# Optimization experiments

Measured on AMD Instinct MI355X. Metric: run time of the kernel, lower is better.

The kernel has to match this reference:

```python
import jax, jax.numpy as jnp
import numpy as np

FEAT_STRIDE = 16
NEG_OV, POS_OV = 0.3, 0.7
RPN_BATCH = 256
NUM_FG = int(0.5 * RPN_BATCH)  # RPN_FG_FRACTION * RPN_BATCHSIZE


def _gen_anchors(base=16, ratios=(0.5, 1.0, 2.0), scales=(4, 8, 16)):
    # 3D extension of the classic generate_anchors: ratio warps w/h, scale multiplies all dims
    ctr = (base - 1) / 2.0
    rows = []
    for r in ratios:
        for s in scales:
            w = base * s * np.sqrt(1.0 / r)
            h = base * s * np.sqrt(r)
            d = float(base * s)
            rows.append([ctr - 0.5 * (w - 1), ctr - 0.5 * (h - 1),
                         ctr + 0.5 * (w - 1), ctr + 0.5 * (h - 1),
                         ctr - 0.5 * (d - 1), ctr + 0.5 * (d - 1)])
    return np.asarray(rows, np.float32)


def setup_inputs() -> dict:
    key = jax.random.key(0)
    ks = jax.random.split(key, 8)
    B, H, W, D, K, A = 2, 48, 48, 24, 20, 9
    cls = jax.random.normal(ks[0], (B, 2 * A, H, W, D), jnp.float32)
    x1 = jax.random.uniform(ks[1], (B, K)) * 600.0
    y1 = jax.random.uniform(ks[2], (B, K)) * 600.0
    z1 = jax.random.uniform(ks[3], (B, K)) * 300.0
    whd = 16.0 + jax.random.uniform(ks[4], (B, K, 3)) * jnp.array([104.0, 104.0, 48.0])
    x2 = jnp.minimum(x1 + whd[..., 0], 767.0)
    y2 = jnp.minimum(y1 + whd[..., 1], 767.0)
    z2 = jnp.minimum(z1 + whd[..., 2], 383.0)
    cid = jax.random.randint(ks[5], (B, K), 1, 4).astype(jnp.float32)
    gt_boxes = jnp.stack([x1, y1, x2, y2, z1, z2, cid], axis=2)
    im_info = jnp.tile(jnp.array([[768.0, 768.0, 384.0]], jnp.float32), (B, 1))
    total = H * W * D * A
    return {
        'rpn_cls_score': cls,
        'gt_boxes': gt_boxes,
        'im_info': im_info,
        'num_boxes': jnp.full((B,), K, jnp.int32),
        'anchors': jnp.asarray(_gen_anchors()),
        'rand_fg': jax.random.uniform(ks[6], (B, total)),
        'rand_bg': jax.random.uniform(ks[7], (B, total)),
    }


def _overlaps(anc, gt):
    # anc: (N,6) [x1,y1,x2,y2,z1,z2]; gt: (B,K,7) -> IoU (B,N,K)
    aw = anc[:, 2] - anc[:, 0] + 1.0
    ah = anc[:, 3] - anc[:, 1] + 1.0
    ad = anc[:, 5] - anc[:, 4] + 1.0
    a_area = aw * ah * ad  # (N,)
    gw = gt[:, :, 2] - gt[:, :, 0] + 1.0
    gh = gt[:, :, 3] - gt[:, :, 1] + 1.0
    gd = gt[:, :, 5] - gt[:, :, 4] + 1.0
    g_area = gw * gh * gd  # (B,K)
    iw = jnp.clip(jnp.minimum(anc[None, :, None, 2], gt[:, None, :, 2]) -
                  jnp.maximum(anc[None, :, None, 0], gt[:, None, :, 0]) + 1.0, 0.0)
    ih = jnp.clip(jnp.minimum(anc[None, :, None, 3], gt[:, None, :, 3]) -
                  jnp.maximum(anc[None, :, None, 1], gt[:, None, :, 1]) + 1.0, 0.0)
    idp = jnp.clip(jnp.minimum(anc[None, :, None, 5], gt[:, None, :, 5]) -
                   jnp.maximum(anc[None, :, None, 4], gt[:, None, :, 4]) + 1.0, 0.0)
    inter = iw * ih * idp
    ov = inter / (a_area[None, :, None] + g_area[:, None, :] - inter)
    gt_zero = (gw == 1.0) & (gh == 1.0) & (gd == 1.0)
    a_zero = (aw == 1.0) & (ah == 1.0) & (ad == 1.0)
    ov = jnp.where(gt_zero[:, None, :], 0.0, ov)
    ov = jnp.where(a_zero[None, :, None], -1.0, ov)
    return ov


def _transform(ex, gt):
    # ex: (N,6); gt: (B,N,6) -> (B,N,6) targets (dx,dy,dz,dw,dh,dd)
    ew = ex[:, 2] - ex[:, 0] + 1.0
    eh = ex[:, 3] - ex[:, 1] + 1.0
    ed = ex[:, 5] - ex[:, 4] + 1.0
    ecx = ex[:, 0] + 0.5 * (ew - 1.0)
    ecy = ex[:, 1] + 0.5 * (eh - 1.0)
    ecz = ex[:, 4] + 0.5 * (ed - 1.0)
    gw = gt[:, :, 2] - gt[:, :, 0] + 1.0
    gh = gt[:, :, 3] - gt[:, :, 1] + 1.0
    gd = gt[:, :, 5] - gt[:, :, 4] + 1.0
    gcx = gt[:, :, 0] + 0.5 * (gw - 1.0)
    gcy = gt[:, :, 1] + 0.5 * (gh - 1.0)
    gcz = gt[:, :, 4] + 0.5 * (gd - 1.0)
    return jnp.stack([(gcx - ecx[None]) / ew[None],
                      (gcy - ecy[None]) / eh[None],
                      (gcz - ecz[None]) / ed[None],
                      jnp.log(gw / ew[None]),
                      jnp.log(gh / eh[None]),
                      jnp.log(gd / ed[None])], axis=2)


def _rank(p):
    # rank of each element when sorted by descending priority, per row
    return jnp.argsort(jnp.argsort(-p, axis=1), axis=1)


def reference(rpn_cls_score, gt_boxes, im_info, num_boxes, anchors, rand_fg, rand_bg):
    B = gt_boxes.shape[0]
    H, W, D = rpn_cls_score.shape[2], rpn_cls_score.shape[3], rpn_cls_score.shape[4]
    A = anchors.shape[0]
    sx = jnp.arange(W, dtype=jnp.float32) * FEAT_STRIDE
    sy = jnp.arange(H, dtype=jnp.float32) * FEAT_STRIDE
    sz = jnp.arange(D, dtype=jnp.float32) * FEAT_STRIDE
    mx, my, mz = jnp.meshgrid(sx, sy, sz, indexing='xy')  # (H,W,D) each
    shifts = jnp.stack([mx.ravel(), my.ravel(), mx.ravel(), my.ravel(), mz.ravel(), mz.ravel()], axis=1)
    all_anchors = (anchors[None, :, :] + shifts[:, None, :]).reshape(-1, 6)  # (total,6)
    total = all_anchors.shape[0]
    inside = ((all_anchors[:, 0] >= 0) & (all_anchors[:, 1] >= 0) & (all_anchors[:, 4] >= 0) &
              (all_anchors[:, 2] < im_info[0, 1]) & (all_anchors[:, 3] < im_info[0, 0]) &
              (all_anchors[:, 5] < im_info[0, 2]))  # (total,)

    ov = _overlaps(all_anchors, gt_boxes)                       # (B,total,K)
    ov_m = jnp.where(inside[None, :, None], ov, -1.0)           # mask outside anchors
    max_ov = ov_m.max(axis=2)
    argmax_ov = jnp.argmax(ov_m, axis=2)                        # (B,total)

    labels = jnp.full((B, total), -1.0, jnp.float32)
    ins = inside[None, :]
    labels = jnp.where(ins & (max_ov < NEG_OV), 0.0, labels)
    gt_max = ov_m.max(axis=1)                                   # (B,K)
    gt_max = jnp.where(gt_max == 0.0, 1e-5, gt_max)
    tie = jnp.sum(ov_m == gt_max[:, None, :], axis=2) > 0
    labels = jnp.where(ins & tie, 1.0, labels)
    labels = jnp.where(ins & (max_ov >= POS_OV), 1.0, labels)

    # fg subsampling: randomly keep at most NUM_FG positives per image
    fg = labels == 1.0
    rk = _rank(jnp.where(fg, rand_fg, -1.0))
    labels = jnp.where(fg & (rk >= NUM_FG), -1.0, labels)
    # bg subsampling: keep RPN_BATCH - num_fg negatives per image
    num_bg = RPN_BATCH - jnp.sum(labels == 1.0, axis=1)         # (B,)
    bg = labels == 0.0
    rkb = _rank(jnp.where(bg, rand_bg, -1.0))
    labels = jnp.where(bg & (rkb >= num_bg[:, None]), -1.0, labels)

    assigned = jnp.take_along_axis(gt_boxes, argmax_ov[:, :, None], axis=1)  # (B,total,7)
    bbox_targets = _transform(all_anchors, assigned[:, :, :6])
    bbox_targets = jnp.where(inside[None, :, None], bbox_targets, 0.0)

    in_w = jnp.where(labels == 1.0, 1.0, 0.0)                   # RPN_BBOX_INSIDE_WEIGHTS[0]=1
    # replicate original bug: weights from the LAST image's example count
    num_examples = jnp.sum(labels[-1] >= 0.0).astype(jnp.float32)
    w = 1.0 / num_examples
    out_w = jnp.where(labels == 1.0, w, jnp.where(labels == 0.0, w, 0.0))

    labels_o = labels.reshape(B, H, W, D, A).transpose(0, 4, 1, 2, 3).reshape(B, 1, A * H * D, W)
    bt_o = bbox_targets.reshape(B, H, W, D, A * 6).transpose(0, 4, 1, 2, 3)
    iw_o = jnp.broadcast_to(in_w[:, :, None], (B, total, 6)).reshape(B, H, W, D, 6 * A).transpose(0, 4, 1, 2, 3)
    ow_o = jnp.broadcast_to(out_w[:, :, None], (B, total, 6)).reshape(B, H, W, D, 6 * A).transpose(0, 4, 1, 2, 3)
    return labels_o, bt_o, iw_o, ow_o
```

## Files before the change

### kernel.cpp

```cpp
#include <hip/hip_runtime.h>
#include <math.h>

#define BB 2
#define HH 48
#define WW 48
#define DD 24
#define KK 20
#define AA 9
#define TOTAL (HH*WW*DD*AA)
#define SPAT (HH*WW*DD)
#define OUT0N (BB*TOTAL)
#define CH 54
#define NB 4096
#define CAPB 256
#define FG_QUOTA 128
#define RPN_B 256
#define STRIDE_F 16.0f

#define O_REC    0
#define O_GTMAX  (OUT0N)
#define O_HIST   (O_GTMAX + BB*KK)
#define O_CUT    (O_HIST + 4*NB)
#define O_W      (O_CUT + 16)
#define O_LIST   (O_W + 1)

__device__ __forceinline__ unsigned enc_f(float f){
  unsigned u = __float_as_uint(f);
  return (u & 0x80000000u) ? ~u : (u | 0x80000000u);
}
__device__ __forceinline__ float dec_f(unsigned u){
  return (u & 0x80000000u) ? __uint_as_float(u & 0x7FFFFFFFu) : __uint_as_float(~u);
}
#define ENC_NEG1 0x407FFFFFu

__device__ __forceinline__ float iou_pre(float ax1,float ay1,float ax2,float ay2,
                                         float az1,float az2,float a_area,
                                         const float* g){
  #pragma clang fp contract(off)
  float iw = fminf(ax2,g[2]) - fmaxf(ax1,g[0]) + 1.0f; iw = fmaxf(iw,0.0f);
  float ih = fminf(ay2,g[3]) - fmaxf(ay1,g[1]) + 1.0f; ih = fmaxf(ih,0.0f);
  float id = fminf(az2,g[5]) - fmaxf(az1,g[4]) + 1.0f; id = fmaxf(id,0.0f);
  float inter = iw*ih*id;
  if (inter <= 0.0f) return 0.0f;
  return inter / ((a_area + g[6]) - inter);
}

__device__ __forceinline__ void gt_derive(const float* gt7, float* g8){
  #pragma clang fp contract(off)
  float gw = gt7[2]-gt7[0]+1.0f, gh = gt7[3]-gt7[1]+1.0f, gd = gt7[5]-gt7[4]+1.0f;
  g8[0]=gt7[0]; g8[1]=gt7[1]; g8[2]=gt7[2]; g8[3]=gt7[3];
  g8[4]=gt7[4]; g8[5]=gt7[5]; g8[6]=gw*gh*gd; g8[7]=0.0f;
}

#define GM_SB 108
__global__ void __launch_bounds__(256) k_gtmax(const float* __restrict__ gt,
    const float* __restrict__ anc, const float* __restrict__ imi,
    unsigned* __restrict__ ws){
  __shared__ float s_gd[KK*8];
  __shared__ float s_a6[6];
  __shared__ float s_im[3];
  __shared__ unsigned s_max[KK];
  int tid = threadIdx.x;
  int a = blockIdx.y;
  int b = blockIdx.z;
  if (b == 0 && a == 0 && blockIdx.x < 16){
    int base = blockIdx.x*256 + tid;
    #pragma unroll
    for (int j=0;j<4;j++) ws[O_HIST + j*NB + base] = 0u;
  }
  if (tid < KK) gt_derive(&gt[(b*KK+tid)*7], &s_gd[tid*8]);
  if (tid < 6)  s_a6[tid] = anc[a*6+tid];
  if (tid < 3)  s_im[tid] = imi[tid];
  if (tid < KK) s_max[tid] = ENC_NEG1;
  __syncthreads();
  float rmax[KK];
  #pragma unroll
  for (int k=0;k<KK;k++) rmax[k] = -1.0f;
  int s0 = blockIdx.x*256 + tid;
  #pragma unroll
  for (int j=0; j<2; j++){
    int s = s0 + j*(GM_SB*256);
    int d = s % DD; int s2 = s / DD;
    int w = s2 % WW; int h = s2 / WW;
    float fx = w*STRIDE_F, fy = h*STRIDE_F, fz = d*STRIDE_F;
    float ax1=s_a6[0]+fx, ay1=s_a6[1]+fy, ax2=s_a6[2]+fx;
    float ay2=s_a6[3]+fy, az1=s_a6[4]+fz, az2=s_a6[5]+fz;
    bool inside = (ax1>=0.f)&&(ay1>=0.f)&&(az1>=0.f)&&
                  (ax2<s_im[1])&&(ay2<s_im[0])&&(az2<s_im[2]);
    if (inside){
      #pragma clang fp contract(off)
      float aw = ax2-ax1+1.0f, ah = ay2-ay1+1.0f, ad = az2-az1+1.0f;
      float a_area = aw*ah*ad;
      #pragma unroll
      for (int k=0;k<KK;k++)
        rmax[k] = fmaxf(rmax[k], iou_pre(ax1,ay1,ax2,ay2,az1,az2,a_area,&s_gd[k*8]));
    }
  }
  #pragma unroll
  for (int k=0;k<KK;k++){
    float v = rmax[k];
    for (int off=32; off>0; off>>=1) v = fmaxf(v, __shfl_down(v, off, 64));
    if ((tid & 63) == 0) atomicMax(&s_max[k], enc_f(v));
  }
  __syncthreads();
  if (tid < KK) atomicMax(&ws[O_GTMAX + b*KK + tid], s_max[tid]);
}

__global__ void __launch_bounds__(256) k_label(const float* __restrict__ gt,
    const float* __restrict__ anc, const float* __restrict__ imi,
    const float* __restrict__ rfg, const float* __restrict__ rbg,
    unsigned* __restrict__ ws){
  __shared__ float s_gd[BB*KK*8];
  __shared__ float s_anc[AA*6];
  __shared__ float s_im[3];
  __shared__ float s_gm[BB*KK];
  int tid = threadIdx.x;
  int t = blockIdx.x*256 + tid;
  int d = t % DD; int r1 = t/DD;
  int w = r1 % WW; int r2 = r1/WW;
  int h = r2 % HH; int r3 = r2/HH;
  int a = r3 % AA; int b = r3/AA;
  int i = ((h*WW+w)*DD + d)*AA + a;
  float rf = rfg[b*TOTAL + i];
  float rb = rbg[b*TOTAL + i];
  if (tid < BB*KK) gt_derive(&gt[tid*7], &s_gd[tid*8]);
  for (int j=tid; j<AA*6; j+=256) s_anc[j] = anc[j];
  if (tid<3) s_im[tid] = imi[tid];
  if (tid<BB*KK){ float g = dec_f(ws[O_GTMAX+tid]); if (g==0.0f) g = 1e-5f; s_gm[tid]=g; }
  __syncthreads();
  float fx=w*STRIDE_F, fy=h*STRIDE_F, fz=d*STRIDE_F;
  float ax1=s_anc[a*6+0]+fx, ay1=s_anc[a*6+1]+fy, ax2=s_anc[a*6+2]+fx;
  float ay2=s_anc[a*6+3]+fy, az1=s_anc[a*6+4]+fz, az2=s_anc[a*6+5]+fz;
  bool inside = (ax1>=0.f)&&(ay1>=0.f)&&(az1>=0.f)&&
                (ax2<s_im[1])&&(ay2<s_im[0])&&(az2<s_im[2]);
  float L = -1.0f;
  int am = 0;
  if (inside){
    #pragma clang fp contract(off)
    float aw = ax2-ax1+1.0f, ah = ay2-ay1+1.0f, ad = az2-az1+1.0f;
    float a_area = aw*ah*ad;
    float mv = -2.0f; bool tie = false;
    #pragma unroll
    for (int k=0;k<KK;k++){
      float ov = iou_pre(ax1,ay1,ax2,ay2,az1,az2,a_area,&s_gd[(b*KK+k)*8]);
      if (ov > mv){ mv = ov; am = k; }
      tie = tie || (ov == s_gm[b*KK+k]);
    }
    if (mv < 0.3f) L = 0.0f;
    if (tie)       L = 1.0f;
    if (mv >= 0.7f) L = 1.0f;
  }
  unsigned code = (L==1.0f) ? 2u : ((L==0.0f) ? 1u : 0u);
  unsigned bucket = 0;
  if (code){
    int fl = (code==1u ? 2 : 0) + b;
    float r = (code==1u) ? rb : rf;
    bucket = (unsigned)min(NB-1, (int)(r*(float)NB));
    unsigned pos = atomicAdd(&ws[O_HIST + fl*NB + bucket], 1u);
    if (pos < CAPB) ((int*)ws)[O_LIST + ((fl*NB + (int)bucket)<<8) + pos] = i;
  }
  ws[O_REC + t] = code | ((unsigned)am<<2) | (bucket<<7);
}

__global__ void __launch_bounds__(256) k_cuts(unsigned* __restrict__ ws){
  int fl = blockIdx.x; int tid = threadIdx.x;
  int b = fl & 1; int isbg = fl >> 1;
  const int CHK = NB/256;
  __shared__ unsigned ps[256];
  __shared__ unsigned s_fg;
  if (tid == 0) s_fg = 0u;
  __syncthreads();
  int hi = NB - CHK*tid;
  unsigned hv[CHK];
  #pragma unroll
  for (int e=0; e<CHK; e++) hv[e] = ws[O_HIST + fl*NB + (hi-CHK+e)];
  unsigned part = 0;
  #pragma unroll
  for (int e=0; e<CHK; e++) part += hv[e];
  if (isbg){
    unsigned fv[CHK];
    #pragma unroll
    for (int e=0; e<CHK; e++) fv[e] = ws[O_HIST + b*NB + tid*CHK + e];
    unsigned pf = 0;
    #pragma unroll
    for (int e=0; e<CHK; e++) pf += fv[e];
    atomicAdd(&s_fg, pf);
  }
  ps[tid] = part;
  __syncthreads();
  for (int off=1; off<256; off<<=1){
    unsigned v = (tid>=off) ? ps[tid-off] : 0u;
    __syncthreads();
    ps[tid] += v;
    __syncthreads();
  }
  unsigned N = ps[255];
  unsigned excl = ps[tid] - part;
  unsigned F = isbg ? s_fg : N;
  int quota = isbg ? (RPN_B - (int)min(F, (unsigned)FG_QUOTA)) : FG_QUOTA;
  if (fl == 3 && tid == 0){
    int fgk = min((int)F, FG_QUOTA);
    int bgk = min((int)N, RPN_B - fgk);
    ((float*)ws)[O_W] = 1.0f / (float)(fgk + bgk);
  }
  int* cut = (int*)&ws[O_CUT + fl*4];
  if ((int)N <= quota){
    if (tid==0){ cut[0] = -1; cut[1] = 0; cut[2] = quota; cut[3] = 0; }
    return;
  }
  unsigned cum = excl;
  #pragma unroll
  for (int e=CHK-1; e>=0; e--){
    int bk = hi-CHK+e;
    unsigned c = hv[e];
    if (c > 0u && (unsigned)(quota-1) >= cum && (unsigned)(quota-1) < cum + c){
      cut[0] = bk; cut[1] = (int)cum; cut[2] = quota; cut[3] = (int)c;
    }
    cum += c;
  }
}

__global__ void __launch_bounds__(256) k_out(const float* __restrict__ gt,
    const float* __restrict__ anc, const float* __restrict__ imi,
    const float* __restrict__ rfg, const float* __restrict__ rbg,
    float* __restrict__ out, const unsigned* __restrict__ ws){
  __shared__ float s_gt[BB*KK*7];
  __shared__ float s_anc[AA*6];
  __shared__ float s_im[3];
  __shared__ float s_w;
  int tid = threadIdx.x;
  for (int j=tid; j<BB*KK*7; j+=256) s_gt[j] = gt[j];
  for (int j=tid; j<AA*6; j+=256) s_anc[j] = anc[j];
  if (tid<3) s_im[tid] = imi[tid];
  if (tid==0) s_w = ((const float*)ws)[O_W];
  __syncthreads();
  int t4 = (blockIdx.x*256 + tid)*4;
  int d0 = t4 % DD; int r1=t4/DD;
  int w = r1 % WW; int r2 = r1/WW;
  int h = r2 % HH; int r3 = r2/HH;
  int a = r3 % AA; int b = r3/AA;
  const uint4 rec4 = *reinterpret_cast<const uint4*>(&ws[O_REC + t4]);
  unsigned recs[4] = {rec4.x, rec4.y, rec4.z, rec4.w};
  float sw = s_w;
  float fx=w*STRIDE_F, fy=h*STRIDE_F;
  float ax1=s_anc[a*6+0]+fx, ay1=s_anc[a*6+1]+fy;
  float ax2=s_anc[a*6+2]+fx, ay2=s_anc[a*6+3]+fy;
  float L4[4], iw4[4], ow4[4], btv[6][4];
  #pragma unroll
  for (int dd=0; dd<4; dd++){
    int d = d0 + dd;
    unsigned rec = recs[dd];
    unsigned code = rec & 3u;
    int am = (int)((rec>>2) & 31u);
    int bucket = (int)((rec>>7) & 4095u);
    float L = (code==2u) ? 1.0f : ((code==1u) ? 0.0f : -1.0f);
    if (code){
      int isbg = (code==1u);
      int fl = isbg*2 + b;
      const int* cut = (const int*)&ws[O_CUT + fl*4];
      int cutb = cut[0];
      if (cutb >= 0){
        if (bucket < cutb) L = -1.0f;
        else if (bucket == cutb){
          int rank_base = cut[1], quota = cut[2];
          int n = min(cut[3], CAPB);
          int i = ((h*WW+w)*DD + d)*AA + a;
          const float* ra = isbg ? rbg : rfg;
          float ri = ra[b*TOTAL + i];
          const int* lst = (const int*)ws + O_LIST + ((fl*NB + cutb)<<8);
          int cnt = 0;
          for (int e=0; e<n; e++){
            int jj = lst[e];
            float rj = ra[b*TOTAL + jj];
            cnt += (rj > ri) || (rj == ri && jj < i);
          }
          if (rank_base + cnt >= quota) L = -1.0f;
        }
      }
    }
    float fz = d*STRIDE_F;
    float az1 = s_anc[a*6+4]+fz, az2 = s_anc[a*6+5]+fz;
    bool inside = (ax1>=0.f)&&(ay1>=0.f)&&(az1>=0.f)&&
                  (ax2<s_im[1])&&(ay2<s_im[0])&&(az2<s_im[2]);
    float bt[6] = {0.f,0.f,0.f,0.f,0.f,0.f};
    if (inside){
      const float* g = &s_gt[(b*KK + am)*7];
      float ew=ax2-ax1+1.f, eh=ay2-ay1+1.f, ed=az2-az1+1.f;
      float ecx=ax1+0.5f*(ew-1.f), ecy=ay1+0.5f*(eh-1.f), ecz=az1+0.5f*(ed-1.f);
      float gw=g[2]-g[0]+1.f, gh=g[3]-g[1]+1.f, gd=g[5]-g[4]+1.f;
      float gcx=g[0]+0.5f*(gw-1.f), gcy=g[1]+0.5f*(gh-1.f), gcz=g[4]+0.5f*(gd-1.f);
      bt[0]=(gcx-ecx)/ew; bt[1]=(gcy-ecy)/eh; bt[2]=(gcz-ecz)/ed;
      bt[3]=logf(gw/ew);  bt[4]=logf(gh/eh);  bt[5]=logf(gd/ed);
    }
    L4[dd] = L;
    iw4[dd] = (L==1.0f) ? 1.0f : 0.0f;
    ow4[dd] = (L==1.0f || L==0.0f) ? sw : 0.0f;
    #pragma unroll
    for (int c=0; c<6; c++) btv[c][dd] = bt[c];
  }
  *reinterpret_cast<float4*>(&out[t4]) = make_float4(L4[0],L4[1],L4[2],L4[3]);
  int sp = (h*WW + w)*DD + d0;
  float* out1 = out + OUT0N;
  float* out2 = out1 + BB*CH*SPAT;
  float* out3 = out2 + BB*CH*SPAT;
  int basech = (b*CH + a*6)*SPAT + sp;
  float4 iwv = make_float4(iw4[0],iw4[1],iw4[2],iw4[3]);
  float4 owv = make_float4(ow4[0],ow4[1],ow4[2],ow4[3]);
  #pragma unroll
  for (int c=0; c<6; c++){
    int off = basech + c*SPAT;
    *reinterpret_cast<float4*>(&out1[off]) = make_float4(btv[c][0],btv[c][1],btv[c][2],btv[c][3]);
    *reinterpret_cast<float4*>(&out2[off]) = iwv;
    *reinterpret_cast<float4*>(&out3[off]) = owv;
  }
}

extern "C" void kernel_launch(void* const* d_in, const int* in_sizes, int n_in,
                              void* d_out, int out_size, void* d_ws, size_t ws_size,
                              hipStream_t stream) {
  (void)in_sizes; (void)n_in; (void)out_size; (void)ws_size;
  const float* gt  = (const float*)d_in[1];
  const float* imi = (const float*)d_in[2];
  const float* anc = (const float*)d_in[4];
  const float* rfg = (const float*)d_in[5];
  const float* rbg = (const float*)d_in[6];
  float* out = (float*)d_out;
  unsigned* ws = (unsigned*)d_ws;
  int nb = (OUT0N + 255)/256;
  int nb4 = (OUT0N + 1023)/1024;
  hipMemsetAsync((char*)d_ws + (size_t)O_GTMAX*4, 0, BB*KK*4, stream);
  k_gtmax <<<dim3(GM_SB, AA, BB), dim3(256), 0, stream>>>(gt, anc, imi, ws);
  k_label <<<dim3(nb), dim3(256), 0, stream>>>(gt, anc, imi, rfg, rbg, ws);
  k_cuts  <<<dim3(4), dim3(256), 0, stream>>>(ws);
  k_out   <<<dim3(nb4), dim3(256), 0, stream>>>(gt, anc, imi, rfg, rbg, out, ws);
}
```

Before: 191.2 us.

## Fuse all four stages into one cooperative kernel with grid syncs

Replaces the memset plus four kernel launches with a single cooperative kernel of 972 blocks. Each thread handles four anchors and keeps its records in registers across grid.sync barriers, so the intermediate record array is no longer written and read back. The per-GT max now uses per-block partials instead of global atomics, and the IoU is computed twice inside the fused kernel. The cost is several grid-wide barriers, a 256-register budget from launch_bounds(256,4), and a fallback to the old launches if the cooperative launch fails.

Result: slower. 592.4 us (+209.9%).

```diff
diff --git a/kernel.cpp b/kernel.cpp
--- a/kernel.cpp
+++ b/kernel.cpp
@@ -1,5 +1,8 @@
 #include <hip/hip_runtime.h>
+#include <hip/hip_cooperative_groups.h>
 #include <math.h>
+
+namespace cg = cooperative_groups;
 
 #define BB 2
 #define HH 48
@@ -16,6 +19,8 @@
 #define FG_QUOTA 128
 #define RPN_B 256
 #define STRIDE_F 16.0f
+#define GRID 972
+#define NBLK_B 486
 
 #define O_REC    0
 #define O_GTMAX  (OUT0N)
@@ -23,6 +28,7 @@
 #define O_CUT    (O_HIST + 4*NB)
 #define O_W      (O_CUT + 16)
 #define O_LIST   (O_W + 1)
+#define O_PART   (O_LIST + 4*NB*CAPB)
 
 __device__ __forceinline__ unsigned enc_f(float f){
   unsigned u = __float_as_uint(f);
@@ -50,6 +56,256 @@
   float gw = gt7[2]-gt7[0]+1.0f, gh = gt7[3]-gt7[1]+1.0f, gd = gt7[5]-gt7[4]+1.0f;
   g8[0]=gt7[0]; g8[1]=gt7[1]; g8[2]=gt7[2]; g8[3]=gt7[3];
   g8[4]=gt7[4]; g8[5]=gt7[5]; g8[6]=gw*gh*gd; g8[7]=0.0f;
+}
+
+__global__ void __launch_bounds__(256, 4) k_fused(
+    const float* __restrict__ gt, const float* __restrict__ anc,
+    const float* __restrict__ imi, const float* __restrict__ rfg,
+    const float* __restrict__ rbg, float* __restrict__ out,
+    unsigned* __restrict__ ws){
+  cg::grid_group grid = cg::this_grid();
+  float* ws_f = (float*)ws;
+  __shared__ float s_gd[BB*KK*8];
+  __shared__ float s_anc[AA*6];
+  __shared__ float s_im[3];
+  __shared__ float s_gm[BB*KK];
+  __shared__ float s_red[4][KK];
+  __shared__ unsigned ps[256];
+  __shared__ unsigned s_fg;
+  __shared__ float s_w;
+  int tid = threadIdx.x;
+  int blk = blockIdx.x;
+  int wv = tid >> 6, ln = tid & 63;
+  int t4 = (blk*256 + tid)*4;
+  int d0 = t4 % DD; int r1 = t4/DD;
+  int w  = r1 % WW; int r2 = r1/WW;
+  int h  = r2 % HH; int r3 = r2/HH;
+  int a  = r3 % AA; int b  = r3/AA;
+  if (tid < BB*KK) gt_derive(&gt[tid*7], &s_gd[tid*8]);
+  for (int j=tid; j<AA*6; j+=256) s_anc[j] = anc[j];
+  if (tid < 3) s_im[tid] = imi[tid];
+  if (blk < 16){
+    int base = blk*256 + tid;
+    #pragma unroll
+    for (int j=0;j<4;j++) ws[O_HIST + j*NB + base] = 0u;
+  }
+  __syncthreads();
+  float fx = w*STRIDE_F, fy = h*STRIDE_F;
+  float ax1=s_anc[a*6+0]+fx, ay1=s_anc[a*6+1]+fy;
+  float ax2=s_anc[a*6+2]+fx, ay2=s_anc[a*6+3]+fy;
+  float anz1 = s_anc[a*6+4], anz2 = s_anc[a*6+5];
+  bool okxy = (ax1>=0.f)&&(ay1>=0.f)&&(ax2<s_im[1])&&(ay2<s_im[0]);
+  float rmax[KK];
+  #pragma unroll
+  for (int k=0;k<KK;k++) rmax[k] = -1.0f;
+  #pragma unroll
+  for (int dd=0; dd<4; dd++){
+    float fz = (float)(d0+dd)*STRIDE_F;
+    float az1 = anz1+fz, az2 = anz2+fz;
+    bool inside = okxy && (az1>=0.f) && (az2<s_im[2]);
+    if (inside){
+      #pragma clang fp contract(off)
+      float aw = ax2-ax1+1.0f, ah = ay2-ay1+1.0f, ad = az2-az1+1.0f;
+      float a_area = aw*ah*ad;
+      #pragma unroll
+      for (int k=0;k<KK;k++)
+        rmax[k] = fmaxf(rmax[k], iou_pre(ax1,ay1,ax2,ay2,az1,az2,a_area,&s_gd[(b*KK+k)*8]));
+    }
+  }
+  #pragma unroll
+  for (int k=0;k<KK;k++){
+    float v = rmax[k];
+    #pragma unroll
+    for (int off=32; off>0; off>>=1) v = fmaxf(v, __shfl_down(v, off, 64));
+    if (ln == 0) s_red[wv][k] = v;
+  }
+  __syncthreads();
+  if (tid < KK)
+    ws_f[O_PART + blk*KK + tid] = fmaxf(fmaxf(s_red[0][tid],s_red[1][tid]),
+                                        fmaxf(s_red[2][tid],s_red[3][tid]));
+  grid.sync();
+  if (blk < BB*KK){
+    int bb = blk / KK, k = blk % KK;
+    float m = -1.0f;
+    for (int j=tid; j<NBLK_B; j+=256)
+      m = fmaxf(m, ws_f[O_PART + (bb*NBLK_B + j)*KK + k]);
+    #pragma unroll
+    for (int off=32; off>0; off>>=1) m = fmaxf(m, __shfl_down(m, off, 64));
+    if (ln == 0) s_red[wv][0] = m;
+    __syncthreads();
+    if (tid == 0){
+      float g = fmaxf(fmaxf(s_red[0][0],s_red[1][0]), fmaxf(s_red[2][0],s_red[3][0]));
+      if (g == 0.0f) g = 1e-5f;
+      ws_f[O_GTMAX + blk] = g;
+    }
+  }
+  grid.sync();
+  if (tid < BB*KK) s_gm[tid] = ws_f[O_GTMAX + tid];
+  __syncthreads();
+  int ibase = ((h*WW + w)*DD + d0)*AA + a;
+  float rfv[4], rbv[4];
+  #pragma unroll
+  for (int dd=0; dd<4; dd++){
+    rfv[dd] = rfg[b*TOTAL + ibase + dd*AA];
+    rbv[dd] = rbg[b*TOTAL + ibase + dd*AA];
+  }
+  unsigned recs[4];
+  #pragma unroll
+  for (int dd=0; dd<4; dd++){
+    float fz = (float)(d0+dd)*STRIDE_F;
+    float az1 = anz1+fz, az2 = anz2+fz;
+    bool inside = okxy && (az1>=0.f) && (az2<s_im[2]);
+    float L = -1.0f; int am = 0;
+    if (inside){
+      #pragma clang fp contract(off)
+      float aw = ax2-ax1+1.0f, ah = ay2-ay1+1.0f, ad = az2-az1+1.0f;
+      float a_area = aw*ah*ad;
+      float mv = -2.0f; bool tie = false;
+      #pragma unroll
+      for (int k=0;k<KK;k++){
+        float ov = iou_pre(ax1,ay1,ax2,ay2,az1,az2,a_area,&s_gd[(b*KK+k)*8]);
+        if (ov > mv){ mv = ov; am = k; }
+        tie = tie || (ov == s_gm[b*KK+k]);
+      }
+      if (mv < 0.3f) L = 0.0f;
+      if (tie)       L = 1.0f;
+      if (mv >= 0.7f) L = 1.0f;
+    }
+    unsigned code = (L==1.0f) ? 2u : ((L==0.0f) ? 1u : 0u);
+    unsigned bucket = 0;
+    if (code){
+      int fl = (code==1u ? 2 : 0) + b;
+      float r = (code==1u) ? rbv[dd] : rfv[dd];
+      bucket = (unsigned)min(NB-1, (int)(r*(float)NB));
+      unsigned pos = atomicAdd(&ws[O_HIST + fl*NB + bucket], 1u);
+      if (pos < CAPB) ((int*)ws)[O_LIST + ((fl*NB + (int)bucket)<<8) + pos] = ibase + dd*AA;
+    }
+    recs[dd] = code | ((unsigned)am<<2) | (bucket<<7);
+  }
+  grid.sync();
+  if (blk < 4){
+    int fl = blk;
+    int bq = fl & 1; int isbg = fl >> 1;
+    const int CHK = NB/256;
+    if (tid == 0) s_fg = 0u;
+    __syncthreads();
+    int hi = NB - CHK*tid;
+    unsigned hv[16];
+    #pragma unroll
+    for (int e=0; e<CHK; e++) hv[e] = ws[O_HIST + fl*NB + (hi-CHK+e)];
+    unsigned part = 0;
+    #pragma unroll
+    for (int e=0; e<CHK; e++) part += hv[e];
+    if (isbg){
+      unsigned pf = 0;
+      #pragma unroll
+      for (int e=0; e<CHK; e++) pf += ws[O_HIST + bq*NB + tid*CHK + e];
+      atomicAdd(&s_fg, pf);
+    }
+    ps[tid] = part;
+    __syncthreads();
+    for (int off=1; off<256; off<<=1){
+      unsigned v = (tid>=off) ? ps[tid-off] : 0u;
+      __syncthreads();
+      ps[tid] += v;
+      __syncthreads();
+    }
+    unsigned N = ps[255];
+    unsigned excl = ps[tid] - part;
+    unsigned F = isbg ? s_fg : N;
+    int quota = isbg ? (RPN_B - (int)min(F, (unsigned)FG_QUOTA)) : FG_QUOTA;
+    if (fl == 3 && tid == 0){
+      int fgk = min((int)F, FG_QUOTA);
+      int bgk = min((int)N, RPN_B - fgk);
+      ws_f[O_W] = 1.0f / (float)(fgk + bgk);
+    }
+    int* cut = (int*)&ws[O_CUT + fl*4];
+    if ((int)N <= quota){
+      if (tid==0){ cut[0] = -1; cut[1] = 0; cut[2] = quota; cut[3] = 0; }
+    } else {
+      unsigned cum = excl;
+      #pragma unroll
+      for (int e=CHK-1; e>=0; e--){
+        int bk = hi-CHK+e;
+        unsigned c = hv[e];
+        if (c > 0u && (unsigned)(quota-1) >= cum && (unsigned)(quota-1) < cum + c){
+          cut[0] = bk; cut[1] = (int)cum; cut[2] = quota; cut[3] = (int)c;
+        }
+        cum += c;
+      }
+    }
+  }
+  grid.sync();
+  if (tid == 0) s_w = ws_f[O_W];
+  __syncthreads();
+  float sw = s_w;
+  float L4[4], iw4[4], ow4[4], btv[6][4];
+  #pragma unroll
+  for (int dd=0; dd<4; dd++){
+    int d = d0 + dd;
+    unsigned rec = recs[dd];
+    unsigned code = rec & 3u;
+    int am = (int)((rec>>2) & 31u);
+    int bucket = (int)((rec>>7) & 4095u);
+    float L = (code==2u) ? 1.0f : ((code==1u) ? 0.0f : -1.0f);
+    if (code){
+      int isbg = (code==1u);
+      int fl = isbg*2 + b;
+      const int* cut = (const int*)&ws[O_CUT + fl*4];
+      int cutb = cut[0];
+      if (cutb >= 0){
+        if (bucket < cutb) L = -1.0f;
+        else if (bucket == cutb){
+          int rank_base = cut[1], quota = cut[2];
+          int n = min(cut[3], CAPB);
+          int i = ibase + dd*AA;
+          const float* ra = isbg ? rbg : rfg;
+          float ri = isbg ? rbv[dd] : rfv[dd];
+          const int* lst = (const int*)ws + O_LIST + ((fl*NB + cutb)<<8);
+          int cnt = 0;
+          for (int e=0; e<n; e++){
+            int jj = lst[e];
+            float rj = ra[b*TOTAL + jj];
+            cnt += (rj > ri) || (rj == ri && jj < i);
+          }
+          if (rank_base + cnt >= quota) L = -1.0f;
+        }
+      }
+    }
+    float fz = (float)d*STRIDE_F;
+    float az1 = anz1+fz, az2 = anz2+fz;
+    bool inside = okxy && (az1>=0.f) && (az2<s_im[2]);
+    float bt[6] = {0.f,0.f,0.f,0.f,0.f,0.f};
+    if (inside){
+      const float* g = &s_gd[(b*KK + am)*8];
+      float ew=ax2-ax1+1.f, eh=ay2-ay1+1.f, ed=az2-az1+1.f;
+      float ecx=ax1+0.5f*(ew-1.f), ecy=ay1+0.5f*(eh-1.f), ecz=az1+0.5f*(ed-1.f);
+      float gw=g[2]-g[0]+1.f, gh=g[3]-g[1]+1.f, gdd=g[5]-g[4]+1.f;
+      float gcx=g[0]+0.5f*(gw-1.f), gcy=g[1]+0.5f*(gh-1.f), gcz=g[4]+0.5f*(gdd-1.f);
+      bt[0]=(gcx-ecx)/ew; bt[1]=(gcy-ecy)/eh; bt[2]=(gcz-ecz)/ed;
+      bt[3]=logf(gw/ew);  bt[4]=logf(gh/eh);  bt[5]=logf(gdd/ed);
+    }
+    L4[dd] = L;
+    iw4[dd] = (L==1.0f) ? 1.0f : 0.0f;
+    ow4[dd] = (L==1.0f || L==0.0f) ? sw : 0.0f;
+    #pragma unroll
+    for (int c=0; c<6; c++) btv[c][dd] = bt[c];
+  }
+  *reinterpret_cast<float4*>(&out[t4]) = make_float4(L4[0],L4[1],L4[2],L4[3]);
+  int sp = (h*WW + w)*DD + d0;
+  float* out1 = out + OUT0N;
+  float* out2 = out1 + BB*CH*SPAT;
+  float* out3 = out2 + BB*CH*SPAT;
+  int basech = (b*CH + a*6)*SPAT + sp;
+  float4 iwv = make_float4(iw4[0],iw4[1],iw4[2],iw4[3]);
+  float4 owv = make_float4(ow4[0],ow4[1],ow4[2],ow4[3]);
+  #pragma unroll
+  for (int c=0; c<6; c++){
+    int off = basech + c*SPAT;
+    *reinterpret_cast<float4*>(&out1[off]) = make_float4(btv[c][0],btv[c][1],btv[c][2],btv[c][3]);
+    *reinterpret_cast<float4*>(&out2[off]) = iwv;
+    *reinterpret_cast<float4*>(&out3[off]) = owv;
+  }
 }
 
 #define GM_SB 108
@@ -103,7 +359,10 @@
     if ((tid & 63) == 0) atomicMax(&s_max[k], enc_f(v));
   }
   __syncthreads();
-  if (tid < KK) atomicMax(&ws[O_GTMAX + b*KK + tid], s_max[tid]);
+  if (tid < KK){
+    unsigned e = s_max[tid];
+    if (e > ws[O_GTMAX + b*KK + tid]) atomicMax(&ws[O_GTMAX + b*KK + tid], e);
+  }
 }
 
 __global__ void __launch_bounds__(256) k_label(const float* __restrict__ gt,
@@ -171,19 +430,16 @@
   if (tid == 0) s_fg = 0u;
   __syncthreads();
   int hi = NB - CHK*tid;
-  unsigned hv[CHK];
+  unsigned hv[16];
   #pragma unroll
   for (int e=0; e<CHK; e++) hv[e] = ws[O_HIST + fl*NB + (hi-CHK+e)];
   unsigned part = 0;
   #pragma unroll
   for (int e=0; e<CHK; e++) part += hv[e];
   if (isbg){
-    unsigned fv[CHK];
-    #pragma unroll
-    for (int e=0; e<CHK; e++) fv[e] = ws[O_HIST + b*NB + tid*CHK + e];
     unsigned pf = 0;
     #pragma unroll
-    for (int e=0; e<CHK; e++) pf += fv[e];
+    for (int e=0; e<CHK; e++) pf += ws[O_HIST + b*NB + tid*CHK + e];
     atomicAdd(&s_fg, pf);
   }
   ps[tid] = part;
@@ -326,11 +582,18 @@
   const float* rbg = (const float*)d_in[6];
   float* out = (float*)d_out;
   unsigned* ws = (unsigned*)d_ws;
-  int nb = (OUT0N + 255)/256;
-  int nb4 = (OUT0N + 1023)/1024;
-  hipMemsetAsync((char*)d_ws + (size_t)O_GTMAX*4, 0, BB*KK*4, stream);
-  k_gtmax <<<dim3(GM_SB, AA, BB), dim3(256), 0, stream>>>(gt, anc, imi, ws);
-  k_label <<<dim3(nb), dim3(256), 0, stream>>>(gt, anc, imi, rfg, rbg, ws);
-  k_cuts  <<<dim3(4), dim3(256), 0, stream>>>(ws);
-  k_out   <<<dim3(nb4), dim3(256), 0, stream>>>(gt, anc, imi, rfg, rbg, out, ws);
-}
+
+  void* args[] = {(void*)&gt, (void*)&anc, (void*)&imi, (void*)&rfg,
+                  (void*)&rbg, (void*)&out, (void*)&ws};
+  hipError_t e = hipLaunchCooperativeKernel((void*)k_fused, dim3(GRID),
+                                            dim3(256), args, 0, stream);
+  if (e != hipSuccess){
+    int nb = (OUT0N + 255)/256;
+    int nb4 = (OUT0N + 1023)/1024;
+    hipMemsetAsync((char*)d_ws + (size_t)O_GTMAX*4, 0, BB*KK*4, stream);
+    k_gtmax <<<dim3(GM_SB, AA, BB), dim3(256), 0, stream>>>(gt, anc, imi, ws);
+    k_label <<<dim3(nb), dim3(256), 0, stream>>>(gt, anc, imi, rfg, rbg, ws);
+    k_cuts  <<<dim3(4), dim3(256), 0, stream>>>(ws);
+    k_out   <<<dim3(nb4), dim3(256), 0, stream>>>(gt, anc, imi, rfg, rbg, out, ws);
+  }
+}
```

## Replace atomic gt-max with per-block partials and process four anchors per thread

Applied to the files above, without the earlier changes.

k_gtmax now computes four anchors per thread with GT boxes read directly from global, and writes per-block partial maxima to a workspace array instead of using encoded atomicMax plus a memset. k_label reduces those partials itself, then handles four consecutive depth positions per thread, reusing the GT loads and the x/y inside test and writing records as a vector store. The aim is to cut atomics, shared-memory setup, one memset launch and redundant GT loads. The cost is a redundant partial reduction in every k_label block and higher register pressure.

Result: no change. 189.4 us (-0.9%).

```diff
diff --git a/kernel.cpp b/kernel.cpp
--- a/kernel.cpp
+++ b/kernel.cpp
@@ -16,6 +16,8 @@
 #define FG_QUOTA 128
 #define RPN_B 256
 #define STRIDE_F 16.0f
+#define K1_SB 54
+#define NPART (AA*K1_SB)
 
 #define O_REC    0
 #define O_GTMAX  (OUT0N)
@@ -23,143 +25,166 @@
 #define O_CUT    (O_HIST + 4*NB)
 #define O_W      (O_CUT + 16)
 #define O_LIST   (O_W + 1)
-
-__device__ __forceinline__ unsigned enc_f(float f){
-  unsigned u = __float_as_uint(f);
-  return (u & 0x80000000u) ? ~u : (u | 0x80000000u);
-}
-__device__ __forceinline__ float dec_f(unsigned u){
-  return (u & 0x80000000u) ? __uint_as_float(u & 0x7FFFFFFFu) : __uint_as_float(~u);
-}
-#define ENC_NEG1 0x407FFFFFu
-
-__device__ __forceinline__ float iou_pre(float ax1,float ay1,float ax2,float ay2,
+#define O_PART   (O_LIST + 4*NB*CAPB)
+
+struct GtRec { float x1,y1,x2,y2,z1,z2,area; };
+__device__ __forceinline__ GtRec gt_load(const float* __restrict__ gt, int b, int k){
+  #pragma clang fp contract(off)
+  const float* p = &gt[(b*KK+k)*7];
+  GtRec g;
+  g.x1=p[0]; g.y1=p[1]; g.x2=p[2]; g.y2=p[3]; g.z1=p[4]; g.z2=p[5];
+  float gw = g.x2-g.x1+1.0f, gh = g.y2-g.y1+1.0f, gd = g.z2-g.z1+1.0f;
+  g.area = gw*gh*gd;
+  return g;
+}
+
+__device__ __forceinline__ float iou_rec(float ax1,float ay1,float ax2,float ay2,
                                          float az1,float az2,float a_area,
-                                         const float* g){
+                                         const GtRec& g){
   #pragma clang fp contract(off)
-  float iw = fminf(ax2,g[2]) - fmaxf(ax1,g[0]) + 1.0f; iw = fmaxf(iw,0.0f);
-  float ih = fminf(ay2,g[3]) - fmaxf(ay1,g[1]) + 1.0f; ih = fmaxf(ih,0.0f);
-  float id = fminf(az2,g[5]) - fmaxf(az1,g[4]) + 1.0f; id = fmaxf(id,0.0f);
+  float iw = fminf(ax2,g.x2) - fmaxf(ax1,g.x1) + 1.0f; iw = fmaxf(iw,0.0f);
+  float ih = fminf(ay2,g.y2) - fmaxf(ay1,g.y1) + 1.0f; ih = fmaxf(ih,0.0f);
+  float id = fminf(az2,g.z2) - fmaxf(az1,g.z1) + 1.0f; id = fmaxf(id,0.0f);
   float inter = iw*ih*id;
   if (inter <= 0.0f) return 0.0f;
-  return inter / ((a_area + g[6]) - inter);
-}
-
-__device__ __forceinline__ void gt_derive(const float* gt7, float* g8){
-  #pragma clang fp contract(off)
-  float gw = gt7[2]-gt7[0]+1.0f, gh = gt7[3]-gt7[1]+1.0f, gd = gt7[5]-gt7[4]+1.0f;
-  g8[0]=gt7[0]; g8[1]=gt7[1]; g8[2]=gt7[2]; g8[3]=gt7[3];
-  g8[4]=gt7[4]; g8[5]=gt7[5]; g8[6]=gw*gh*gd; g8[7]=0.0f;
-}
-
-#define GM_SB 108
+  return inter / ((a_area + g.area) - inter);
+}
+
 __global__ void __launch_bounds__(256) k_gtmax(const float* __restrict__ gt,
     const float* __restrict__ anc, const float* __restrict__ imi,
     unsigned* __restrict__ ws){
-  __shared__ float s_gd[KK*8];
-  __shared__ float s_a6[6];
-  __shared__ float s_im[3];
-  __shared__ unsigned s_max[KK];
+  float* ws_f = (float*)ws;
+  __shared__ float s_red[4][KK];
   int tid = threadIdx.x;
-  int a = blockIdx.y;
-  int b = blockIdx.z;
-  if (b == 0 && a == 0 && blockIdx.x < 16){
+  int wv = tid>>6, ln = tid&63;
+  int a = blockIdx.y, b = blockIdx.z;
+  if (b==0 && a==0 && blockIdx.x<16){
     int base = blockIdx.x*256 + tid;
     #pragma unroll
     for (int j=0;j<4;j++) ws[O_HIST + j*NB + base] = 0u;
   }
-  if (tid < KK) gt_derive(&gt[(b*KK+tid)*7], &s_gd[tid*8]);
-  if (tid < 6)  s_a6[tid] = anc[a*6+tid];
-  if (tid < 3)  s_im[tid] = imi[tid];
-  if (tid < KK) s_max[tid] = ENC_NEG1;
-  __syncthreads();
-  float rmax[KK];
-  #pragma unroll
-  for (int k=0;k<KK;k++) rmax[k] = -1.0f;
+  float im0=imi[0], im1=imi[1], im2=imi[2];
+  float a0=anc[a*6+0], a1=anc[a*6+1], a2=anc[a*6+2];
+  float a3=anc[a*6+3], a4=anc[a*6+4], a5=anc[a*6+5];
   int s0 = blockIdx.x*256 + tid;
-  #pragma unroll
-  for (int j=0; j<2; j++){
-    int s = s0 + j*(GM_SB*256);
-    int d = s % DD; int s2 = s / DD;
-    int w = s2 % WW; int h = s2 / WW;
-    float fx = w*STRIDE_F, fy = h*STRIDE_F, fz = d*STRIDE_F;
-    float ax1=s_a6[0]+fx, ay1=s_a6[1]+fy, ax2=s_a6[2]+fx;
-    float ay2=s_a6[3]+fy, az1=s_a6[4]+fz, az2=s_a6[5]+fz;
-    bool inside = (ax1>=0.f)&&(ay1>=0.f)&&(az1>=0.f)&&
-                  (ax2<s_im[1])&&(ay2<s_im[0])&&(az2<s_im[2]);
-    if (inside){
+  float X1[4],Y1[4],X2[4],Y2[4],Z1[4],Z2[4],AR[4];
+  bool OK[4];
+  #pragma unroll
+  for (int j=0;j<4;j++){
+    int s = s0 + j*(K1_SB*256);
+    int d = s % DD; int s2 = s/DD; int w = s2%WW; int h = s2/WW;
+    float fx=w*STRIDE_F, fy=h*STRIDE_F, fz=d*STRIDE_F;
+    X1[j]=a0+fx; Y1[j]=a1+fy; X2[j]=a2+fx; Y2[j]=a3+fy; Z1[j]=a4+fz; Z2[j]=a5+fz;
+    OK[j] = (X1[j]>=0.f)&&(Y1[j]>=0.f)&&(Z1[j]>=0.f)&&
+            (X2[j]<im1)&&(Y2[j]<im0)&&(Z2[j]<im2);
+    {
       #pragma clang fp contract(off)
-      float aw = ax2-ax1+1.0f, ah = ay2-ay1+1.0f, ad = az2-az1+1.0f;
-      float a_area = aw*ah*ad;
-      #pragma unroll
-      for (int k=0;k<KK;k++)
-        rmax[k] = fmaxf(rmax[k], iou_pre(ax1,ay1,ax2,ay2,az1,az2,a_area,&s_gd[k*8]));
+      float aw=X2[j]-X1[j]+1.0f, ah=Y2[j]-Y1[j]+1.0f, ad=Z2[j]-Z1[j]+1.0f;
+      AR[j]=aw*ah*ad;
     }
   }
   #pragma unroll
   for (int k=0;k<KK;k++){
-    float v = rmax[k];
-    for (int off=32; off>0; off>>=1) v = fmaxf(v, __shfl_down(v, off, 64));
-    if ((tid & 63) == 0) atomicMax(&s_max[k], enc_f(v));
-  }
-  __syncthreads();
-  if (tid < KK) atomicMax(&ws[O_GTMAX + b*KK + tid], s_max[tid]);
+    GtRec g = gt_load(gt,b,k);
+    float m = -1.0f;
+    #pragma unroll
+    for (int j=0;j<4;j++)
+      if (OK[j]) m = fmaxf(m, iou_rec(X1[j],Y1[j],X2[j],Y2[j],Z1[j],Z2[j],AR[j],g));
+    #pragma unroll
+    for (int off=32; off>0; off>>=1) m = fmaxf(m, __shfl_down(m, off, 64));
+    if (ln==0) s_red[wv][k]=m;
+  }
+  __syncthreads();
+  if (tid<KK){
+    float m = fmaxf(fmaxf(s_red[0][tid],s_red[1][tid]),
+                    fmaxf(s_red[2][tid],s_red[3][tid]));
+    ws_f[O_PART + (b*KK+tid)*NPART + a*K1_SB + blockIdx.x] = m;
+  }
 }
 
 __global__ void __launch_bounds__(256) k_label(const float* __restrict__ gt,
     const float* __restrict__ anc, const float* __restrict__ imi,
     const float* __restrict__ rfg, const float* __restrict__ rbg,
     unsigned* __restrict__ ws){
-  __shared__ float s_gd[BB*KK*8];
-  __shared__ float s_anc[AA*6];
-  __shared__ float s_im[3];
-  __shared__ float s_gm[BB*KK];
+  float* ws_f = (float*)ws;
+  __shared__ float s_gm[KK];
   int tid = threadIdx.x;
-  int t = blockIdx.x*256 + tid;
-  int d = t % DD; int r1 = t/DD;
-  int w = r1 % WW; int r2 = r1/WW;
-  int h = r2 % HH; int r3 = r2/HH;
-  int a = r3 % AA; int b = r3/AA;
-  int i = ((h*WW+w)*DD + d)*AA + a;
-  float rf = rfg[b*TOTAL + i];
-  float rb = rbg[b*TOTAL + i];
-  if (tid < BB*KK) gt_derive(&gt[tid*7], &s_gd[tid*8]);
-  for (int j=tid; j<AA*6; j+=256) s_anc[j] = anc[j];
-  if (tid<3) s_im[tid] = imi[tid];
-  if (tid<BB*KK){ float g = dec_f(ws[O_GTMAX+tid]); if (g==0.0f) g = 1e-5f; s_gm[tid]=g; }
-  __syncthreads();
-  float fx=w*STRIDE_F, fy=h*STRIDE_F, fz=d*STRIDE_F;
-  float ax1=s_anc[a*6+0]+fx, ay1=s_anc[a*6+1]+fy, ax2=s_anc[a*6+2]+fx;
-  float ay2=s_anc[a*6+3]+fy, az1=s_anc[a*6+4]+fz, az2=s_anc[a*6+5]+fz;
-  bool inside = (ax1>=0.f)&&(ay1>=0.f)&&(az1>=0.f)&&
-                (ax2<s_im[1])&&(ay2<s_im[0])&&(az2<s_im[2]);
-  float L = -1.0f;
-  int am = 0;
-  if (inside){
-    #pragma clang fp contract(off)
-    float aw = ax2-ax1+1.0f, ah = ay2-ay1+1.0f, ad = az2-az1+1.0f;
-    float a_area = aw*ah*ad;
-    float mv = -2.0f; bool tie = false;
-    #pragma unroll
-    for (int k=0;k<KK;k++){
-      float ov = iou_pre(ax1,ay1,ax2,ay2,az1,az2,a_area,&s_gd[(b*KK+k)*8]);
-      if (ov > mv){ mv = ov; am = k; }
-      tie = tie || (ov == s_gm[b*KK+k]);
-    }
-    if (mv < 0.3f) L = 0.0f;
-    if (tie)       L = 1.0f;
-    if (mv >= 0.7f) L = 1.0f;
-  }
-  unsigned code = (L==1.0f) ? 2u : ((L==0.0f) ? 1u : 0u);
-  unsigned bucket = 0;
-  if (code){
-    int fl = (code==1u ? 2 : 0) + b;
-    float r = (code==1u) ? rb : rf;
-    bucket = (unsigned)min(NB-1, (int)(r*(float)NB));
-    unsigned pos = atomicAdd(&ws[O_HIST + fl*NB + bucket], 1u);
-    if (pos < CAPB) ((int*)ws)[O_LIST + ((fl*NB + (int)bucket)<<8) + pos] = i;
-  }
-  ws[O_REC + t] = code | ((unsigned)am<<2) | (bucket<<7);
+  int blk = blockIdx.x;
+  int wv = tid>>6, ln = tid&63;
+  int t4 = (blk*256 + tid)*4;
+  int d0 = t4 % DD; int r1=t4/DD; int w=r1%WW; int r2=r1/WW; int h=r2%HH;
+  int b = blk/486; int a = (blk%486)/54;
+  int ibase = ((h*WW+w)*DD + d0)*AA + a;
+  float rfv[4], rbv[4];
+  #pragma unroll
+  for (int dd=0;dd<4;dd++){
+    rfv[dd] = rfg[b*TOTAL + ibase + dd*AA];
+    rbv[dd] = rbg[b*TOTAL + ibase + dd*AA];
+  }
+  for (int k=wv; k<KK; k+=4){
+    float m = -1.0f;
+    for (int j=ln; j<NPART; j+=64)
+      m = fmaxf(m, ws_f[O_PART + (b*KK+k)*NPART + j]);
+    #pragma unroll
+    for (int off=32; off>0; off>>=1) m = fmaxf(m, __shfl_down(m, off, 64));
+    if (ln==0){ if (m==0.0f) m = 1e-5f; s_gm[k]=m; }
+  }
+  __syncthreads();
+  float im0=imi[0], im1=imi[1], im2=imi[2];
+  float a0=anc[a*6+0], a1=anc[a*6+1], a2=anc[a*6+2];
+  float a3=anc[a*6+3], a4=anc[a*6+4], a5=anc[a*6+5];
+  float fx=w*STRIDE_F, fy=h*STRIDE_F;
+  float ax1=a0+fx, ay1=a1+fy, ax2=a2+fx, ay2=a3+fy;
+  bool okxy = (ax1>=0.f)&&(ay1>=0.f)&&(ax2<im1)&&(ay2<im0);
+  float Z1[4],Z2[4],AR[4]; bool OK[4];
+  #pragma unroll
+  for (int dd=0;dd<4;dd++){
+    float fz = (float)(d0+dd)*STRIDE_F;
+    Z1[dd]=a4+fz; Z2[dd]=a5+fz;
+    OK[dd] = okxy && (Z1[dd]>=0.f) && (Z2[dd]<im2);
+    {
+      #pragma clang fp contract(off)
+      float aw=ax2-ax1+1.0f, ah=ay2-ay1+1.0f, ad=Z2[dd]-Z1[dd]+1.0f;
+      AR[dd]=aw*ah*ad;
+    }
+  }
+  float mv[4]={-2.f,-2.f,-2.f,-2.f};
+  int   am[4]={0,0,0,0};
+  bool  tie[4]={false,false,false,false};
+  #pragma unroll
+  for (int k=0;k<KK;k++){
+    GtRec g = gt_load(gt,b,k);
+    float gmk = s_gm[k];
+    #pragma unroll
+    for (int dd=0;dd<4;dd++){
+      if (OK[dd]){
+        float ov = iou_rec(ax1,ay1,ax2,ay2,Z1[dd],Z2[dd],AR[dd],g);
+        if (ov > mv[dd]){ mv[dd]=ov; am[dd]=k; }
+        tie[dd] = tie[dd] || (ov == gmk);
+      }
+    }
+  }
+  unsigned recs[4];
+  #pragma unroll
+  for (int dd=0;dd<4;dd++){
+    float L = -1.0f;
+    if (OK[dd]){
+      if (mv[dd] < 0.3f) L = 0.0f;
+      if (tie[dd])       L = 1.0f;
+      if (mv[dd] >= 0.7f) L = 1.0f;
+    }
+    unsigned code = (L==1.0f) ? 2u : ((L==0.0f) ? 1u : 0u);
+    unsigned bucket = 0;
+    if (code){
+      int fl = (code==1u ? 2 : 0) + b;
+      float r = (code==1u) ? rbv[dd] : rfv[dd];
+      bucket = (unsigned)min(NB-1, (int)(r*(float)NB));
+      unsigned pos = atomicAdd(&ws[O_HIST + fl*NB + bucket], 1u);
+      if (pos < CAPB) ((int*)ws)[O_LIST + ((fl*NB + (int)bucket)<<8) + pos] = ibase + dd*AA;
+    }
+    recs[dd] = code | ((unsigned)am[dd]<<2) | (bucket<<7);
+  }
+  *reinterpret_cast<uint4*>(&ws[O_REC + t4]) = make_uint4(recs[0],recs[1],recs[2],recs[3]);
 }
 
 __global__ void __launch_bounds__(256) k_cuts(unsigned* __restrict__ ws){
@@ -171,19 +196,16 @@
   if (tid == 0) s_fg = 0u;
   __syncthreads();
   int hi = NB - CHK*tid;
-  unsigned hv[CHK];
+  unsigned hv[16];
   #pragma unroll
   for (int e=0; e<CHK; e++) hv[e] = ws[O_HIST + fl*NB + (hi-CHK+e)];
   unsigned part = 0;
   #pragma unroll
   for (int e=0; e<CHK; e++) part += hv[e];
   if (isbg){
-    unsigned fv[CHK];
-    #pragma unroll
-    for (int e=0; e<CHK; e++) fv[e] = ws[O_HIST + b*NB + tid*CHK + e];
     unsigned pf = 0;
     #pragma unroll
-    for (int e=0; e<CHK; e++) pf += fv[e];
+    for (int e=0; e<CHK; e++) pf += ws[O_HIST + b*NB + tid*CHK + e];
     atomicAdd(&s_fg, pf);
   }
   ps[tid] = part;
@@ -326,11 +348,9 @@
   const float* rbg = (const float*)d_in[6];
   float* out = (float*)d_out;
   unsigned* ws = (unsigned*)d_ws;
-  int nb = (OUT0N + 255)/256;
   int nb4 = (OUT0N + 1023)/1024;
-  hipMemsetAsync((char*)d_ws + (size_t)O_GTMAX*4, 0, BB*KK*4, stream);
-  k_gtmax <<<dim3(GM_SB, AA, BB), dim3(256), 0, stream>>>(gt, anc, imi, ws);
-  k_label <<<dim3(nb), dim3(256), 0, stream>>>(gt, anc, imi, rfg, rbg, ws);
+  k_gtmax <<<dim3(K1_SB, AA, BB), dim3(256), 0, stream>>>(gt, anc, imi, ws);
+  k_label <<<dim3(nb4), dim3(256), 0, stream>>>(gt, anc, imi, rfg, rbg, ws);
   k_cuts  <<<dim3(4), dim3(256), 0, stream>>>(ws);
   k_out   <<<dim3(nb4), dim3(256), 0, stream>>>(gt, anc, imi, rfg, rbg, out, ws);
 }
```
